# Optimization experiments

Measured on AMD Instinct MI355X. Metric: run time of the kernel, lower is better.

## Reference

```python
import jax, jax.numpy as jnp
import numpy as np

B, L, D = 2, 1024, 768
NH, HD = 12, 64
NL = 6
MLP = 3072
THETA = 10000.0


def _rope(pos, dim, theta):
    # pos: (L,) float -> (L, dim//2, 2, 2) rotation matrices (FLUX rope)
    omega = 1.0 / (theta ** (jnp.arange(0, dim, 2, dtype=jnp.float32) / dim))
    out = pos[:, None] * omega  # (L, dim//2)
    cos, sin = jnp.cos(out), jnp.sin(out)
    return jnp.stack([jnp.stack([cos, -sin], -1), jnp.stack([sin, cos], -1)], -2)


def _build_pe(seq_len, pe_dim):
    # 2D spatial ids: axis0 = x (fast), axis1 = y (slow); axes_dim = [pe_dim//2, pe_dim//2]
    h = w = int(seq_len ** 0.5)
    y_ids = jnp.repeat(jnp.arange(h, dtype=jnp.float32), w)
    x_ids = jnp.tile(jnp.arange(w, dtype=jnp.float32), h)
    half = pe_dim // 2
    pe = jnp.concatenate([_rope(x_ids, half, THETA), _rope(y_ids, half, THETA)], axis=-3)
    return pe[None, None]  # (1, 1, L, pe_dim//2, 2, 2)


def _apply_rope(x, pe):
    # x: (B, H, L, HD)
    xs = x.reshape(x.shape[:-1] + (-1, 1, 2))
    out = pe[..., 0] * xs[..., 0] + pe[..., 1] * xs[..., 1]
    return out.reshape(x.shape)


def _rmsnorm(x, scale):
    return x * jax.lax.rsqrt(jnp.mean(x * x, axis=-1, keepdims=True) + 1e-6) * scale


def _layernorm(x, g, b):
    m = jnp.mean(x, axis=-1, keepdims=True)
    v = jnp.var(x, axis=-1, keepdims=True)
    return (x - m) * jax.lax.rsqrt(v + 1e-5) * g + b


def _forward(spatial_features, density_weights, condition_embeddings,
             spatial_w, spatial_b, cond_w, cond_b,
             ln1_g, ln1_b, qkv_w, q_scale, k_scale, proj_w, proj_b,
             dscale, dbias, ln2_g, ln2_b, mlp_w1, mlp_b1, mlp_w2, mlp_b2,
             out_w, out_b):
    Bsz, Ls, Ds = spatial_features.shape
    x = spatial_features @ spatial_w + spatial_b
    x = x + (condition_embeddings @ cond_w + cond_b)[:, None, :]
    pe = _build_pe(Ls, HD)
    dflat = density_weights.reshape(Bsz, 1, Ls)  # H*W == L, no interpolation
    attn_scale = HD ** -0.5
    for i in range(NL):
        h = _layernorm(x, ln1_g[i], ln1_b[i])
        qkv = (h @ qkv_w[i]).reshape(Bsz, Ls, 3, NH, HD).transpose(2, 0, 3, 1, 4)
        q, k, v = qkv[0], qkv[1], qkv[2]
        q = _rmsnorm(q, q_scale[i])
        k = _rmsnorm(k, k_scale[i])
        q = _apply_rope(q, pe)
        k = _apply_rope(k, pe)
        scores = jnp.einsum('bhld,bhmd->bhlm', q, k) * attn_scale
        scores = scores + (dscale[i] * dflat[..., None] + dbias[i])  # (B,1,L,1) bcast
        attn = jax.nn.softmax(scores, axis=-1)
        o = jnp.einsum('bhlm,bhmd->bhld', attn, v)
        o = o.transpose(0, 2, 1, 3).reshape(Bsz, Ls, Ds)
        x = x + o @ proj_w[i] + proj_b[i]
        h2 = _layernorm(x, ln2_g[i], ln2_b[i])
        x = x + jax.nn.gelu(h2 @ mlp_w1[i] + mlp_b1[i], approximate=False) @ mlp_w2[i] + mlp_b2[i]
    return x @ out_w + out_b


def setup_inputs() -> dict:
    key = jax.random.key(0)
    ks = jax.random.split(key, 16)
    s = 0.02
    inp = {
        'spatial_features': jax.random.normal(ks[0], (B, L, D), jnp.float32),
        'density_weights': jax.random.uniform(ks[1], (B, 32, 32), jnp.float32),
        'condition_embeddings': jax.random.normal(ks[2], (B, 1536), jnp.float32),
        'spatial_w': jax.random.normal(ks[3], (D, D), jnp.float32) * s,
        'spatial_b': jnp.zeros((D,), jnp.float32),
        'cond_w': jax.random.normal(ks[4], (1536, D), jnp.float32) * s,
        'cond_b': jnp.zeros((D,), jnp.float32),
        'ln1_g': jnp.ones((NL, D), jnp.float32),
        'ln1_b': jnp.zeros((NL, D), jnp.float32),
        'qkv_w': jax.random.normal(ks[5], (NL, D, 3 * D), jnp.float32) * s,
        'q_scale': jnp.ones((NL, HD), jnp.float32),
        'k_scale': jnp.ones((NL, HD), jnp.float32),
        'proj_w': jax.random.normal(ks[6], (NL, D, D), jnp.float32) * s,
        'proj_b': jnp.zeros((NL, D), jnp.float32),
        'dscale': jnp.ones((NL,), jnp.float32),
        'dbias': jnp.zeros((NL,), jnp.float32),
        'ln2_g': jnp.ones((NL, D), jnp.float32),
        'ln2_b': jnp.zeros((NL, D), jnp.float32),
        'mlp_w1': jax.random.normal(ks[7], (NL, D, MLP), jnp.float32) * s,
        'mlp_b1': jnp.zeros((NL, MLP), jnp.float32),
        'mlp_w2': jax.random.normal(ks[8], (NL, MLP, D), jnp.float32) * s,
        'mlp_b2': jnp.zeros((NL, D), jnp.float32),
        'out_w': jax.random.normal(ks[9], (D, D), jnp.float32) * s,
        'out_b': jnp.zeros((D,), jnp.float32),
    }
    return inp


def reference(spatial_features, density_weights, condition_embeddings,
              spatial_w, spatial_b, cond_w, cond_b,
              ln1_g, ln1_b, qkv_w, q_scale, k_scale, proj_w, proj_b,
              dscale, dbias, ln2_g, ln2_b, mlp_w1, mlp_b1, mlp_w2, mlp_b2,
              out_w, out_b):
    return _forward(spatial_features, density_weights, condition_embeddings,
                    spatial_w, spatial_b, cond_w, cond_b,
                    ln1_g, ln1_b, qkv_w, q_scale, k_scale, proj_w, proj_b,
                    dscale, dbias, ln2_g, ln2_b, mlp_w1, mlp_b1, mlp_w2, mlp_b2,
                    out_w, out_b)
```

## Files before the change

kernel.cpp:

```cpp
#include <hip/hip_runtime.h>
#include <hip/hip_bf16.h>
#include <cstdint>
#include <cstddef>

typedef unsigned short u16;
using short8  = __attribute__((ext_vector_type(8))) short;
using floatx4 = __attribute__((ext_vector_type(4))) float;

typedef __attribute__((address_space(1))) void gvoid;
typedef __attribute__((address_space(3))) void svoid;

__device__ __forceinline__ u16 f2bf(float f) {
  __hip_bfloat16 h = __float2bfloat16(f);
  return __builtin_bit_cast(u16, h);
}

__device__ __forceinline__ floatx4 mfma16(short8 a, short8 b, floatx4 c) {
  return __builtin_amdgcn_mfma_f32_16x16x32_bf16(a, b, c, 0, 0, 0);
}

__device__ __forceinline__ void glds16(const u16* g, u16* l) {
  __builtin_amdgcn_global_load_lds((gvoid*)g, (svoid*)l, 16, 0, 0);
}

__global__ void pe_kernel(float* __restrict__ pet) {
  int t = blockIdx.x * 256 + threadIdx.x;
  if (t >= 32768) return;
  int l = t >> 5, j = t & 31;
  float pos   = (j < 16) ? (float)(l & 31) : (float)(l >> 5);
  float omega = powf(10000.f, -(float)(j & 15) / 16.f);
  float a = pos * omega;
  pet[2 * t]     = cosf(a);
  pet[2 * t + 1] = sinf(a);
}

__global__ __launch_bounds__(256) void twt_kernel(const float* __restrict__ in,
                                                  u16* __restrict__ out, int K, int N) {
  size_t lofs = (size_t)blockIdx.z * K * N;
  in  += lofs;
  out += lofs;
  __shared__ float tile[32][33];
  int bx = blockIdx.x;
  int by = blockIdx.y;
  int t = threadIdx.x;
  int lk = t >> 3, ln = (t & 7) * 4;
  float4 v = *(const float4*)(in + (size_t)(by * 32 + lk) * N + bx * 32 + ln);
  tile[lk][ln + 0] = v.x; tile[lk][ln + 1] = v.y;
  tile[lk][ln + 2] = v.z; tile[lk][ln + 3] = v.w;
  __syncthreads();
  int n = t >> 3, k0 = (t & 7) * 4;
  ushort4 o;
  o.x = f2bf(tile[k0 + 0][n]); o.y = f2bf(tile[k0 + 1][n]);
  o.z = f2bf(tile[k0 + 2][n]); o.w = f2bf(tile[k0 + 3][n]);
  *(ushort4*)(out + (size_t)(bx * 32 + n) * K + by * 32 + k0) = o;
}

__global__ void cvt_kernel(const float* __restrict__ in, u16* __restrict__ out, int n) {
  int i = blockIdx.x * 256 + threadIdx.x;
  if (i < n) out[i] = f2bf(in[i]);
}

__global__ __launch_bounds__(256) void condp_kernel(const float* __restrict__ ce,
                                                    const float* __restrict__ w,
                                                    float* __restrict__ partial) {
  int d = blockIdx.x * 256 + threadIdx.x;
  int c = blockIdx.y;
  #pragma unroll
  for (int b = 0; b < 2; b++) {
    float acc = 0.f;
    #pragma unroll 4
    for (int k = c * 96; k < c * 96 + 96; k++) acc += ce[b * 1536 + k] * w[(size_t)k * 768 + d];
    partial[(size_t)(c * 2 + b) * 768 + d] = acc;
  }
}

__global__ __launch_bounds__(256) void condr_kernel(const float* __restrict__ partial,
                                                    const float* __restrict__ bias,
                                                    float* __restrict__ out) {
  int t = blockIdx.x * 256 + threadIdx.x;
  int b = t / 768, d = t % 768;
  float acc = bias[d];
  #pragma unroll
  for (int c = 0; c < 16; c++) acc += partial[(size_t)(c * 2 + b) * 768 + d];
  out[b * 768 + d] = acc;
}

__global__ __launch_bounds__(256) void ln_kernel(const float* __restrict__ x,
                                                 const float* __restrict__ g,
                                                 const float* __restrict__ b,
                                                 u16* __restrict__ out) {
  int row = blockIdx.x;
  const float* xr = x + (size_t)row * 768;
  int t = threadIdx.x;
  float v0 = xr[t], v1 = xr[t + 256], v2 = xr[t + 512];
  float s = v0 + v1 + v2, s2 = v0 * v0 + v1 * v1 + v2 * v2;
  #pragma unroll
  for (int o = 32; o >= 1; o >>= 1) { s += __shfl_xor(s, o); s2 += __shfl_xor(s2, o); }
  __shared__ float red[8];
  int w = t >> 6, lane = t & 63;
  if (lane == 0) { red[w] = s; red[4 + w] = s2; }
  __syncthreads();
  s  = red[0] + red[1] + red[2] + red[3];
  s2 = red[4] + red[5] + red[6] + red[7];
  float mean = s * (1.f / 768.f);
  float var  = s2 * (1.f / 768.f) - mean * mean;
  float rstd = rsqrtf(var + 1e-5f);
  u16* orow = out + (size_t)row * 768;
  orow[t]       = f2bf((v0 - mean) * rstd * g[t] + b[t]);
  orow[t + 256] = f2bf((v1 - mean) * rstd * g[t + 256] + b[t + 256]);
  orow[t + 512] = f2bf((v2 - mean) * rstd * g[t + 512] + b[t + 512]);
}

__global__ __launch_bounds__(256) void ropeq_kernel(const float* __restrict__ qkv,
                                                    const float* __restrict__ qs,
                                                    const float* __restrict__ ks,
                                                    const float* __restrict__ pet,
                                                    u16* __restrict__ qb, u16* __restrict__ kb) {
  int gid = blockIdx.x * 4 + (threadIdx.x >> 6);
  int lane = threadIdx.x & 63;
  int h = gid % 12, bl = gid / 12;
  int l = bl & 1023, b = bl >> 10;
  const float* qp = qkv + ((size_t)(b * 1024 + l) * 3 + 0) * 768 + h * 64;
  const float* kp = qp + 768;
  float q = qp[lane], k = kp[lane];
  float sq = q * q, sk = k * k;
  #pragma unroll
  for (int o = 1; o < 64; o <<= 1) { sq += __shfl_xor(sq, o); sk += __shfl_xor(sk, o); }
  q *= rsqrtf(sq * (1.f / 64.f) + 1e-6f) * qs[lane];
  k *= rsqrtf(sk * (1.f / 64.f) + 1e-6f) * ks[lane];
  int j = lane >> 1;
  float c = pet[(l * 32 + j) * 2], s = pet[(l * 32 + j) * 2 + 1];
  float qo = __shfl_xor(q, 1), ko = __shfl_xor(k, 1);
  float qr = (lane & 1) ? (s * qo + c * q) : (c * q - s * qo);
  float kr = (lane & 1) ? (s * ko + c * k) : (c * k - s * ko);
  int bh = b * 12 + h;
  qb[((size_t)bh * 1024 + l) * 64 + lane] = f2bf(qr * 0.125f);
  kb[((size_t)bh * 1024 + l) * 64 + lane] = f2bf(kr);
}

__global__ __launch_bounds__(256) void vtrans_kernel(const float* __restrict__ qkv,
                                                     u16* __restrict__ vt) {
  int lt = blockIdx.x, bh = blockIdx.y;
  int b = bh / 12, h = bh % 12;
  __shared__ float tile[64][65];
  int t = threadIdx.x, c = t & 63, r0 = t >> 6;
  #pragma unroll
  for (int p = 0; p < 16; p++) {
    int lr = p * 4 + r0;
    tile[lr][c] = qkv[((size_t)(b * 1024 + lt * 64 + lr) * 3 + 2) * 768 + h * 64 + c];
  }
  __syncthreads();
  #pragma unroll
  for (int p = 0; p < 16; p++) {
    int d = p * 4 + r0;
    vt[((size_t)bh * 64 + d) * 1024 + lt * 64 + c] = f2bf(tile[c][d]);
  }
}

__global__ __launch_bounds__(256) void attn_split(const u16* __restrict__ qb,
                                                  const u16* __restrict__ kbuf,
                                                  const u16* __restrict__ vt,
                                                  float* __restrict__ po,
                                                  float* __restrict__ pl) {
  const int qt = blockIdx.x, bh = blockIdx.y, sp = blockIdx.z;
  const int lane = threadIdx.x & 63, w = threadIdx.x >> 6;
  const int quad = lane >> 4, l16 = lane & 15;
  __shared__ __align__(16) u16 Ks[128 * 64];
  __shared__ __align__(16) u16 Vs[64 * 128];
  __shared__ __align__(16) u16 Ps[4][16 * 136];
  const u16* Q  = qb   + (size_t)bh * 1024 * 64;
  const u16* Kp = kbuf + (size_t)bh * 1024 * 64;
  const u16* Vp = vt   + (size_t)bh * 64 * 1024;
  const int qrow0 = qt * 64 + w * 16;
  short8 aq0, aq1;
  {
    const u16* qp = Q + (size_t)(qrow0 + l16) * 64 + quad * 8;
    aq0 = *(const short8*)qp;
    aq1 = *(const short8*)(qp + 32);
  }
  floatx4 accO[4];
  #pragma unroll
  for (int i = 0; i < 4; i++) accO[i] = (floatx4){0.f, 0.f, 0.f, 0.f};
  float lsum[4] = {0.f, 0.f, 0.f, 0.f};

  const int krow_in = (lane >> 3);
  const int kchunk  = lane & 7;
  const int vrow_in = (lane >> 4);
  const int vchunk  = lane & 15;

  for (int nt = 0; nt < 4; ++nt) {
    const int kb0 = sp * 512 + nt * 128;
    __syncthreads();
    #pragma unroll
    for (int j = 0; j < 4; j++) {
      int r = w * 32 + j * 8 + krow_in;
      int g = kchunk ^ (r & 7);
      glds16(Kp + (size_t)(kb0 + r) * 64 + g * 8, Ks + (w * 32 + j * 8) * 64);
    }
    #pragma unroll
    for (int j = 0; j < 4; j++) {
      int r = w * 16 + j * 4 + vrow_in;
      int g = vchunk ^ (r & 15);
      glds16(Vp + (size_t)r * 1024 + kb0 + g * 8, Vs + (w * 16 + j * 4) * 128);
    }
    __syncthreads();

    floatx4 s[8];
    #pragma unroll
    for (int n = 0; n < 8; n++) {
      int row = n * 16 + l16;
      int c0 = quad ^ (l16 & 7);
      short8 b0 = *(const short8*)&Ks[row * 64 + c0 * 8];
      short8 b1 = *(const short8*)&Ks[row * 64 + (c0 ^ 4) * 8];
      floatx4 z = (floatx4){0.f, 0.f, 0.f, 0.f};
      z = mfma16(aq0, b0, z);
      s[n] = mfma16(aq1, b1, z);
    }
    #pragma unroll
    for (int n = 0; n < 8; n++) {
      #pragma unroll
      for (int r = 0; r < 4; r++) {
        float pv = __expf(s[n][r] - 8.f);
        lsum[r] += pv;
        Ps[w][(quad * 4 + r) * 136 + n * 16 + l16] = f2bf(pv);
      }
    }
    #pragma unroll
    for (int kt = 0; kt < 4; kt++) {
      short8 ap = *(const short8*)&Ps[w][l16 * 136 + kt * 32 + quad * 8];
      #pragma unroll
      for (int dt = 0; dt < 4; dt++) {
        int vrow = dt * 16 + l16;
        int c = (kt * 4 + quad) ^ l16;
        short8 bv = *(const short8*)&Vs[vrow * 128 + c * 8];
        accO[dt] = mfma16(ap, bv, accO[dt]);
      }
    }
  }
  #pragma unroll
  for (int r = 0; r < 4; r++) {
    #pragma unroll
    for (int o = 1; o < 16; o <<= 1) lsum[r] += __shfl_xor(lsum[r], o);
  }
  const size_t sb = (size_t)(sp * 24 + bh) * 1024;
  #pragma unroll
  for (int r = 0; r < 4; r++) {
    int lr = qrow0 + quad * 4 + r;
    if (l16 == 0) pl[sb + lr] = lsum[r];
    #pragma unroll
    for (int dt = 0; dt < 4; dt++)
      po[(sb + lr) * 64 + dt * 16 + l16] = accO[dt][r];
  }
}

__global__ __launch_bounds__(256) void attn_comb(const float* __restrict__ po,
                                                 const float* __restrict__ pl,
                                                 u16* __restrict__ obuf) {
  int w = threadIdx.x >> 6, lane = threadIdx.x & 63;
  int gr = blockIdx.x * 4 + w;
  int bh = gr >> 10, l = gr & 1023;
  float num = 0.f, den = 0.f;
  #pragma unroll
  for (int s = 0; s < 2; s++) {
    num += po[((size_t)(s * 24 + bh) * 1024 + l) * 64 + lane];
    den += pl[(size_t)(s * 24 + bh) * 1024 + l];
  }
  int b = bh / 12, h = bh % 12;
  obuf[((size_t)(b * 1024 + l)) * 768 + h * 64 + lane] = f2bf(num / den);
}

template <int EPI, int BM, int BN>
__global__ __launch_bounds__(256) void gemm_bt(const u16* __restrict__ A,
                                               const u16* __restrict__ Bt,
                                               const float* __restrict__ bias,
                                               const float* extra,
                                               float* Cf, u16* Cb, int M, int N, int K) {
  constexpr int ROWS = BM + BN;
  constexpr int RPW  = ROWS / 4;
  constexpr int NG   = RPW / 8;
  constexpr int MT   = BM / 32;
  constexpr int NTW  = BN / 32;
  __shared__ __align__(16) u16 S[2][ROWS * 64];
  const int t = threadIdx.x;
  const int lane = t & 63, w = t >> 6;
  const int quad = lane >> 4, l16 = lane & 15;
  const int m0 = blockIdx.y * BM, n0 = blockIdx.x * BN;
  const int wm = (w >> 1) * (BM / 2), wn = (w & 1) * (BN / 2);

  floatx4 acc[MT][NTW];
  #pragma unroll
  for (int i = 0; i < MT; i++)
    #pragma unroll
    for (int j = 0; j < NTW; j++) acc[i][j] = (floatx4){0.f, 0.f, 0.f, 0.f};

  const u16* gsrc[NG];
  int loff[NG];
  #pragma unroll
  for (int j = 0; j < NG; j++) {
    int r = w * RPW + j * 8 + (lane >> 3);
    int c = lane & 7;
    int g = c ^ (r & 7);
    const u16* base = (r < BM) ? (A + (size_t)(m0 + r) * K)
                               : (Bt + (size_t)(n0 + r - BM) * K);
    gsrc[j] = base + g * 8;
    loff[j] = (w * RPW + j * 8) * 64;
  }

  const int NIT = K >> 6;

  auto compute = [&](int buf) {
    const u16* Sb = &S[buf][0];
    #pragma unroll
    for (int kk = 0; kk < 2; kk++) {
      short8 af[MT], bfr[NTW];
      #pragma unroll
      for (int mt = 0; mt < MT; mt++) {
        int ra = wm + mt * 16 + l16;
        af[mt] = *(const short8*)&Sb[ra * 64 + ((((kk << 2) | quad)) ^ (ra & 7)) * 8];
      }
      #pragma unroll
      for (int nt = 0; nt < NTW; nt++) {
        int rb = BM + wn + nt * 16 + l16;
        bfr[nt] = *(const short8*)&Sb[rb * 64 + ((((kk << 2) | quad)) ^ (rb & 7)) * 8];
      }
      #pragma unroll
      for (int mt = 0; mt < MT; mt++)
        #pragma unroll
        for (int nt = 0; nt < NTW; nt++)
          acc[mt][nt] = mfma16(af[mt], bfr[nt], acc[mt][nt]);
    }
  };

  #pragma unroll
  for (int j = 0; j < NG; j++) glds16(gsrc[j], &S[0][loff[j]]);
  __syncthreads();

  int cur = 0;
  for (int it = 0; it < NIT; ++it) {
    if (it + 1 < NIT) {
      #pragma unroll
      for (int j = 0; j < NG; j++) glds16(gsrc[j] + (it + 1) * 64, &S[cur ^ 1][loff[j]]);
    }
    compute(cur);
    if (it + 1 < NIT) __syncthreads();
    cur ^= 1;
  }

  #pragma unroll
  for (int mt = 0; mt < MT; mt++) {
    #pragma unroll
    for (int nt = 0; nt < NTW; nt++) {
      int col = n0 + wn + nt * 16 + l16;
      float bcol = bias ? bias[col] : 0.f;
      #pragma unroll
      for (int r = 0; r < 4; r++) {
        int row = m0 + wm + mt * 16 + quad * 4 + r;
        float v = acc[mt][nt][r] + bcol;
        if (EPI == 1) v += extra[(row >> 10) * N + col];
        if (EPI == 2) v += extra[(size_t)row * N + col];
        if (EPI == 3) v = 0.5f * v * (1.f + erff(v * 0.70710678118654752f));
        if (Cf) Cf[(size_t)row * N + col] = v;
        if (Cb) Cb[(size_t)row * N + col] = f2bf(v);
      }
    }
  }
}

extern "C" void kernel_launch(void* const* d_in, const int* in_sizes, int n_in,
                              void* d_out, int out_size, void* d_ws, size_t ws_size,
                              hipStream_t stream) {
  const float* sf   = (const float*)d_in[0];
  const float* ce   = (const float*)d_in[2];
  const float* sw   = (const float*)d_in[3];
  const float* sb   = (const float*)d_in[4];
  const float* cw   = (const float*)d_in[5];
  const float* cb   = (const float*)d_in[6];
  const float* ln1g = (const float*)d_in[7];
  const float* ln1b = (const float*)d_in[8];
  const float* qkvw = (const float*)d_in[9];
  const float* qsc  = (const float*)d_in[10];
  const float* ksc  = (const float*)d_in[11];
  const float* pw   = (const float*)d_in[12];
  const float* pb   = (const float*)d_in[13];
  const float* ln2g = (const float*)d_in[16];
  const float* ln2b = (const float*)d_in[17];
  const float* w1   = (const float*)d_in[18];
  const float* b1   = (const float*)d_in[19];
  const float* w2   = (const float*)d_in[20];
  const float* b2   = (const float*)d_in[21];
  const float* ow   = (const float*)d_in[22];
  const float* ob   = (const float*)d_in[23];

  char* p = (char*)d_ws;
  auto alloc = [&](size_t bytes) { char* r = p; p += (bytes + 255) & ~(size_t)255; return r; };
  float* pet  = (float*)alloc((size_t)1024 * 32 * 2 * 4);
  u16* swT    = (u16*)alloc((size_t)768 * 768 * 2);
  u16* owT    = (u16*)alloc((size_t)768 * 768 * 2);
  u16* qkvT   = (u16*)alloc((size_t)6 * 2304 * 768 * 2);
  u16* pwT    = (u16*)alloc((size_t)6 * 768 * 768 * 2);
  u16* w1T    = (u16*)alloc((size_t)6 * 3072 * 768 * 2);
  u16* w2T    = (u16*)alloc((size_t)6 * 768 * 3072 * 2);
  u16* sfb    = (u16*)alloc((size_t)2048 * 768 * 2);
  float* cpar = (float*)alloc((size_t)32 * 768 * 4);
  float* cond = (float*)alloc((size_t)2 * 768 * 4);
  float* x    = (float*)alloc((size_t)2048 * 768 * 4);
  u16* xb     = (u16*)alloc((size_t)2048 * 768 * 2);
  u16* h      = (u16*)alloc((size_t)2048 * 768 * 2);
  float* qkv  = (float*)alloc((size_t)2048 * 2304 * 4);
  u16* qbuf   = (u16*)alloc((size_t)2048 * 768 * 2);
  u16* kbuf   = (u16*)alloc((size_t)2048 * 768 * 2);
  u16* vtb    = (u16*)alloc((size_t)2048 * 768 * 2);
  u16* obuf   = (u16*)alloc((size_t)2048 * 768 * 2);
  u16* gbuf   = (u16*)alloc((size_t)2048 * 3072 * 2);
  float* po   = (float*)alloc((size_t)2 * 24 * 1024 * 64 * 4);
  float* pl   = (float*)alloc((size_t)2 * 24 * 1024 * 4);

  pe_kernel<<<128, 256, 0, stream>>>(pet);
  twt_kernel<<<dim3(24, 24, 1), 256, 0, stream>>>(sw, swT, 768, 768);
  twt_kernel<<<dim3(24, 24, 1), 256, 0, stream>>>(ow, owT, 768, 768);
  twt_kernel<<<dim3(72, 24, 6), 256, 0, stream>>>(qkvw, qkvT, 768, 2304);
  twt_kernel<<<dim3(24, 24, 6), 256, 0, stream>>>(pw, pwT, 768, 768);
  twt_kernel<<<dim3(96, 24, 6), 256, 0, stream>>>(w1, w1T, 768, 3072);
  twt_kernel<<<dim3(24, 96, 6), 256, 0, stream>>>(w2, w2T, 3072, 768);
  cvt_kernel<<<(2048 * 768) / 256, 256, 0, stream>>>(sf, sfb, 2048 * 768);
  condp_kernel<<<dim3(3, 16), 256, 0, stream>>>(ce, cw, cpar);
  condr_kernel<<<6, 256, 0, stream>>>(cpar, cb, cond);

  gemm_bt<1, 32, 64><<<dim3(12, 64), 256, 0, stream>>>(sfb, swT, sb, cond, x, nullptr, 2048, 768, 768);

  for (int i = 0; i < 6; i++) {
    ln_kernel<<<2048, 256, 0, stream>>>(x, ln1g + i * 768, ln1b + i * 768, h);
    gemm_bt<0, 32, 128><<<dim3(18, 64), 256, 0, stream>>>(h, qkvT + (size_t)i * 2304 * 768,
                                                          nullptr, nullptr, qkv, nullptr, 2048, 2304, 768);
    ropeq_kernel<<<6144, 256, 0, stream>>>(qkv, qsc + i * 64, ksc + i * 64, pet, qbuf, kbuf);
    vtrans_kernel<<<dim3(16, 24), 256, 0, stream>>>(qkv, vtb);
    attn_split<<<dim3(16, 24, 2), 256, 0, stream>>>(qbuf, kbuf, vtb, po, pl);
    attn_comb<<<6144, 256, 0, stream>>>(po, pl, obuf);
    gemm_bt<2, 32, 64><<<dim3(12, 64), 256, 0, stream>>>(obuf, pwT + (size_t)i * 768 * 768,
                                                         pb + i * 768, x, x, xb, 2048, 768, 768);
    ln_kernel<<<2048, 256, 0, stream>>>(x, ln2g + i * 768, ln2b + i * 768, h);
    gemm_bt<3, 32, 128><<<dim3(24, 64), 256, 0, stream>>>(h, w1T + (size_t)i * 3072 * 768,
                                                          b1 + i * 3072, nullptr, nullptr, gbuf, 2048, 3072, 768);
    gemm_bt<2, 32, 64><<<dim3(12, 64), 256, 0, stream>>>(gbuf, w2T + (size_t)i * 768 * 3072,
                                                         b2 + i * 768, x, x, xb, 2048, 768, 3072);
  }
  gemm_bt<0, 32, 64><<<dim3(12, 64), 256, 0, stream>>>(xb, owT, ob, nullptr, (float*)d_out, nullptr,
                                                       2048, 768, 768);
}
```

Baseline: 1.044 ms.

## Fuse QK RMSNorm+RoPE into QKV GEMM epilogue, triple-buffer GEMM, enlarge tiles

```diff
diff --git a/kernel.cpp b/kernel.cpp
--- a/kernel.cpp
+++ b/kernel.cpp
@@ -111,50 +111,24 @@
   orow[t + 512] = f2bf((v2 - mean) * rstd * g[t + 512] + b[t + 512]);
 }
 
-__global__ __launch_bounds__(256) void ropeq_kernel(const float* __restrict__ qkv,
-                                                    const float* __restrict__ qs,
-                                                    const float* __restrict__ ks,
-                                                    const float* __restrict__ pet,
-                                                    u16* __restrict__ qb, u16* __restrict__ kb) {
-  int gid = blockIdx.x * 4 + (threadIdx.x >> 6);
-  int lane = threadIdx.x & 63;
-  int h = gid % 12, bl = gid / 12;
-  int l = bl & 1023, b = bl >> 10;
-  const float* qp = qkv + ((size_t)(b * 1024 + l) * 3 + 0) * 768 + h * 64;
-  const float* kp = qp + 768;
-  float q = qp[lane], k = kp[lane];
-  float sq = q * q, sk = k * k;
-  #pragma unroll
-  for (int o = 1; o < 64; o <<= 1) { sq += __shfl_xor(sq, o); sk += __shfl_xor(sk, o); }
-  q *= rsqrtf(sq * (1.f / 64.f) + 1e-6f) * qs[lane];
-  k *= rsqrtf(sk * (1.f / 64.f) + 1e-6f) * ks[lane];
-  int j = lane >> 1;
-  float c = pet[(l * 32 + j) * 2], s = pet[(l * 32 + j) * 2 + 1];
-  float qo = __shfl_xor(q, 1), ko = __shfl_xor(k, 1);
-  float qr = (lane & 1) ? (s * qo + c * q) : (c * q - s * qo);
-  float kr = (lane & 1) ? (s * ko + c * k) : (c * k - s * ko);
-  int bh = b * 12 + h;
-  qb[((size_t)bh * 1024 + l) * 64 + lane] = f2bf(qr * 0.125f);
-  kb[((size_t)bh * 1024 + l) * 64 + lane] = f2bf(kr);
-}
-
-__global__ __launch_bounds__(256) void vtrans_kernel(const float* __restrict__ qkv,
-                                                     u16* __restrict__ vt) {
+__global__ __launch_bounds__(256) void vtransb_kernel(const u16* __restrict__ vb,
+                                                      u16* __restrict__ vt) {
   int lt = blockIdx.x, bh = blockIdx.y;
   int b = bh / 12, h = bh % 12;
-  __shared__ float tile[64][65];
-  int t = threadIdx.x, c = t & 63, r0 = t >> 6;
-  #pragma unroll
-  for (int p = 0; p < 16; p++) {
-    int lr = p * 4 + r0;
-    tile[lr][c] = qkv[((size_t)(b * 1024 + lt * 64 + lr) * 3 + 2) * 768 + h * 64 + c];
-  }
+  __shared__ u16 tile[64][72];
+  int t = threadIdx.x;
+  int lr = t >> 2, c0 = (t & 3) * 16;
+  const u16* src = vb + (size_t)(b * 1024 + lt * 64 + lr) * 768 + h * 64 + c0;
+  *(short8*)&tile[lr][c0]     = *(const short8*)src;
+  *(short8*)&tile[lr][c0 + 8] = *(const short8*)(src + 8);
   __syncthreads();
-  #pragma unroll
-  for (int p = 0; p < 16; p++) {
-    int d = p * 4 + r0;
-    vt[((size_t)bh * 64 + d) * 1024 + lt * 64 + c] = f2bf(tile[c][d]);
-  }
+  int d = t >> 2, l0 = (t & 3) * 16;
+  u16 o[16];
+  #pragma unroll
+  for (int i = 0; i < 16; i++) o[i] = tile[l0 + i][d];
+  u16* dst = vt + ((size_t)bh * 64 + d) * 1024 + lt * 64 + l0;
+  *(short8*)dst       = *(short8*)&o[0];
+  *(short8*)(dst + 8) = *(short8*)&o[8];
 }
 
 __global__ __launch_bounds__(256) void attn_split(const u16* __restrict__ qb,
@@ -274,13 +248,16 @@
                                                const u16* __restrict__ Bt,
                                                const float* __restrict__ bias,
                                                const float* extra,
-                                               float* Cf, u16* Cb, int M, int N, int K) {
+                                               float* Cf, u16* Cb, int M, int N, int K,
+                                               const float* qsc, const float* ksc,
+                                               const float* petp,
+                                               u16* qb, u16* kb, u16* vb) {
   constexpr int ROWS = BM + BN;
   constexpr int RPW  = ROWS / 4;
   constexpr int NG   = RPW / 8;
   constexpr int MT   = BM / 32;
   constexpr int NTW  = BN / 32;
-  __shared__ __align__(16) u16 S[2][ROWS * 64];
+  __shared__ __align__(16) u16 S[3][ROWS * 64];
   const int t = threadIdx.x;
   const int lane = t & 63, w = t >> 6;
   const int quad = lane >> 4, l16 = lane & 15;
@@ -333,17 +310,67 @@
 
   #pragma unroll
   for (int j = 0; j < NG; j++) glds16(gsrc[j], &S[0][loff[j]]);
-  __syncthreads();
-
-  int cur = 0;
+  #pragma unroll
+  for (int j = 0; j < NG; j++) glds16(gsrc[j] + 64, &S[1][loff[j]]);
+  asm volatile("s_waitcnt vmcnt(%0)" :: "n"(NG) : "memory");
+  __builtin_amdgcn_s_barrier();
+  asm volatile("" ::: "memory");
+
+  int bufc = 0;
   for (int it = 0; it < NIT; ++it) {
+    if (it + 2 < NIT) {
+      int bufp = bufc + 2; if (bufp >= 3) bufp -= 3;
+      #pragma unroll
+      for (int j = 0; j < NG; j++) glds16(gsrc[j] + (it + 2) * 64, &S[bufp][loff[j]]);
+    }
+    compute(bufc);
     if (it + 1 < NIT) {
-      #pragma unroll
-      for (int j = 0; j < NG; j++) glds16(gsrc[j] + (it + 1) * 64, &S[cur ^ 1][loff[j]]);
-    }
-    compute(cur);
-    if (it + 1 < NIT) __syncthreads();
-    cur ^= 1;
+      if (it + 2 < NIT) asm volatile("s_waitcnt vmcnt(%0)" :: "n"(NG) : "memory");
+      else              asm volatile("s_waitcnt vmcnt(0)" ::: "memory");
+      __builtin_amdgcn_s_barrier();
+      asm volatile("" ::: "memory");
+    }
+    bufc = (bufc + 1 == 3) ? 0 : bufc + 1;
+  }
+
+  if (EPI == 4) {
+    const int cb  = n0 + wn;
+    const int reg = cb / 768;
+    const int hh  = (cb - reg * 768) >> 6;
+    #pragma unroll
+    for (int mt = 0; mt < MT; mt++) {
+      #pragma unroll
+      for (int r = 0; r < 4; r++) {
+        int grow = m0 + wm + mt * 16 + quad * 4 + r;
+        int bI = grow >> 10, lI = grow & 1023;
+        if (reg < 2) {
+          float s2 = 0.f;
+          #pragma unroll
+          for (int nt = 0; nt < NTW; nt++) s2 += acc[mt][nt][r] * acc[mt][nt][r];
+          #pragma unroll
+          for (int o = 1; o < 16; o <<= 1) s2 += __shfl_xor(s2, o);
+          float rstd = rsqrtf(s2 * (1.f / 64.f) + 1e-6f);
+          const float* sc = reg ? ksc : qsc;
+          u16* dst = (reg ? kb : qb) + ((size_t)(bI * 12 + hh) * 1024 + lI) * 64;
+          #pragma unroll
+          for (int nt = 0; nt < NTW; nt++) {
+            int d = nt * 16 + l16;
+            float v = acc[mt][nt][r] * rstd * sc[d];
+            float cv = petp[((lI * 32) + (d >> 1)) * 2];
+            float sv = petp[((lI * 32) + (d >> 1)) * 2 + 1];
+            float ov = __shfl_xor(v, 1);
+            float rv = (d & 1) ? (sv * ov + cv * v) : (cv * v - sv * ov);
+            if (reg == 0) rv *= 0.125f;
+            dst[d] = f2bf(rv);
+          }
+        } else {
+          u16* dst = vb + (size_t)grow * 768 + (cb - 1536);
+          #pragma unroll
+          for (int nt = 0; nt < NTW; nt++) dst[nt * 16 + l16] = f2bf(acc[mt][nt][r]);
+        }
+      }
+    }
+    return;
   }
 
   #pragma unroll
@@ -406,9 +433,9 @@
   float* x    = (float*)alloc((size_t)2048 * 768 * 4);
   u16* xb     = (u16*)alloc((size_t)2048 * 768 * 2);
   u16* h      = (u16*)alloc((size_t)2048 * 768 * 2);
-  float* qkv  = (float*)alloc((size_t)2048 * 2304 * 4);
   u16* qbuf   = (u16*)alloc((size_t)2048 * 768 * 2);
   u16* kbuf   = (u16*)alloc((size_t)2048 * 768 * 2);
+  u16* vb     = (u16*)alloc((size_t)2048 * 768 * 2);
   u16* vtb    = (u16*)alloc((size_t)2048 * 768 * 2);
   u16* obuf   = (u16*)alloc((size_t)2048 * 768 * 2);
   u16* gbuf   = (u16*)alloc((size_t)2048 * 3072 * 2);
@@ -426,24 +453,28 @@
   condp_kernel<<<dim3(3, 16), 256, 0, stream>>>(ce, cw, cpar);
   condr_kernel<<<6, 256, 0, stream>>>(cpar, cb, cond);
 
-  gemm_bt<1, 32, 64><<<dim3(12, 64), 256, 0, stream>>>(sfb, swT, sb, cond, x, nullptr, 2048, 768, 768);
+  gemm_bt<1, 64, 64><<<dim3(12, 32), 256, 0, stream>>>(sfb, swT, sb, cond, x, nullptr,
+      2048, 768, 768, nullptr, nullptr, nullptr, nullptr, nullptr, nullptr);
 
   for (int i = 0; i < 6; i++) {
     ln_kernel<<<2048, 256, 0, stream>>>(x, ln1g + i * 768, ln1b + i * 768, h);
-    gemm_bt<0, 32, 128><<<dim3(18, 64), 256, 0, stream>>>(h, qkvT + (size_t)i * 2304 * 768,
-                                                          nullptr, nullptr, qkv, nullptr, 2048, 2304, 768);
-    ropeq_kernel<<<6144, 256, 0, stream>>>(qkv, qsc + i * 64, ksc + i * 64, pet, qbuf, kbuf);
-    vtrans_kernel<<<dim3(16, 24), 256, 0, stream>>>(qkv, vtb);
+    gemm_bt<4, 64, 128><<<dim3(18, 32), 256, 0, stream>>>(h, qkvT + (size_t)i * 2304 * 768,
+        nullptr, nullptr, nullptr, nullptr, 2048, 2304, 768,
+        qsc + i * 64, ksc + i * 64, pet, qbuf, kbuf, vb);
+    vtransb_kernel<<<dim3(16, 24), 256, 0, stream>>>(vb, vtb);
     attn_split<<<dim3(16, 24, 2), 256, 0, stream>>>(qbuf, kbuf, vtb, po, pl);
     attn_comb<<<6144, 256, 0, stream>>>(po, pl, obuf);
-    gemm_bt<2, 32, 64><<<dim3(12, 64), 256, 0, stream>>>(obuf, pwT + (size_t)i * 768 * 768,
-                                                         pb + i * 768, x, x, xb, 2048, 768, 768);
+    gemm_bt<2, 64, 64><<<dim3(12, 32), 256, 0, stream>>>(obuf, pwT + (size_t)i * 768 * 768,
+        pb + i * 768, x, x, xb, 2048, 768, 768,
+        nullptr, nullptr, nullptr, nullptr, nullptr, nullptr);
     ln_kernel<<<2048, 256, 0, stream>>>(x, ln2g + i * 768, ln2b + i * 768, h);
-    gemm_bt<3, 32, 128><<<dim3(24, 64), 256, 0, stream>>>(h, w1T + (size_t)i * 3072 * 768,
-                                                          b1 + i * 3072, nullptr, nullptr, gbuf, 2048, 3072, 768);
-    gemm_bt<2, 32, 64><<<dim3(12, 64), 256, 0, stream>>>(gbuf, w2T + (size_t)i * 768 * 3072,
-                                                         b2 + i * 768, x, x, xb, 2048, 768, 3072);
-  }
-  gemm_bt<0, 32, 64><<<dim3(12, 64), 256, 0, stream>>>(xb, owT, ob, nullptr, (float*)d_out, nullptr,
-                                                       2048, 768, 768);
-}
+    gemm_bt<3, 64, 128><<<dim3(24, 32), 256, 0, stream>>>(h, w1T + (size_t)i * 3072 * 768,
+        b1 + i * 3072, nullptr, nullptr, gbuf, 2048, 3072, 768,
+        nullptr, nullptr, nullptr, nullptr, nullptr, nullptr);
+    gemm_bt<2, 64, 64><<<dim3(12, 32), 256, 0, stream>>>(gbuf, w2T + (size_t)i * 768 * 3072,
+        b2 + i * 768, x, x, xb, 2048, 768, 3072,
+        nullptr, nullptr, nullptr, nullptr, nullptr, nullptr);
+  }
+  gemm_bt<0, 64, 64><<<dim3(12, 32), 256, 0, stream>>>(xb, owT, ob, nullptr, (float*)d_out, nullptr,
+      2048, 768, 768, nullptr, nullptr, nullptr, nullptr, nullptr, nullptr);
+}
```

Result: faster. 994.4 us (-4.8%).
